# Performance work log

Measured on AMD Instinct MI355X. Metric: run time of the kernel, lower is better.

## Reference

```python
import jax, jax.numpy as jnp
import numpy as np

EMBED_DIM = 768
NUM_HEADS = 12
HEAD_DIM = EMBED_DIM // NUM_HEADS
B, T = 2, 2048


def setup_inputs() -> dict:
    key = jax.random.key(0)
    ks = jax.random.split(key, 11)
    s = 1.0 / np.sqrt(EMBED_DIM)
    return {
        "query": jax.random.normal(ks[0], (B, T, EMBED_DIM), jnp.float32),
        "key_in": jax.random.normal(ks[1], (B, T, EMBED_DIM), jnp.float32),
        "value": jax.random.normal(ks[2], (B, T, EMBED_DIM), jnp.float32),
        "Wq": jax.random.uniform(ks[3], (EMBED_DIM, EMBED_DIM), jnp.float32, -s, s),
        "bq": jnp.zeros((EMBED_DIM,), jnp.float32),
        "Wk": jax.random.uniform(ks[4], (EMBED_DIM, EMBED_DIM), jnp.float32, -s, s),
        "bk": jnp.zeros((EMBED_DIM,), jnp.float32),
        "Wv": jax.random.uniform(ks[5], (EMBED_DIM, EMBED_DIM), jnp.float32, -s, s),
        "bv": jnp.zeros((EMBED_DIM,), jnp.float32),
        "Wo": jax.random.uniform(ks[6], (EMBED_DIM, EMBED_DIM), jnp.float32, -s, s),
        "bo": jnp.zeros((EMBED_DIM,), jnp.float32),
    }


def reference(query, key_in, value, Wq, bq, Wk, bk, Wv, bv, Wo, bo):
    b, t, _ = query.shape

    def split_heads(x):  # [B,T,E] -> [B,H,T,Dh]
        return x.reshape(b, t, NUM_HEADS, HEAD_DIM).transpose(0, 2, 1, 3)

    Q = split_heads(query @ Wq + bq)
    K = split_heads(key_in @ Wk + bk)
    V = split_heads(value @ Wv + bv)

    scores = jnp.einsum("bhqd,bhkd->bhqk", Q, K) / np.sqrt(HEAD_DIM).astype(np.float32)
    attn = jax.nn.softmax(scores, axis=-1)
    out = jnp.einsum("bhqk,bhkd->bhqd", attn, V)  # [B,H,T,Dh]
    out = out.transpose(0, 2, 1, 3).reshape(b, t, EMBED_DIM)
    return out @ Wo + bo
```

## Files before the change

kernel.cpp:

```cpp
#include <hip/hip_runtime.h>
#include <math.h>

typedef __attribute__((ext_vector_type(4))) float  floatx4;
typedef __attribute__((ext_vector_type(8))) short  short8;
typedef __attribute__((ext_vector_type(4))) short  short4v;
typedef __attribute__((ext_vector_type(8))) __bf16 bf16x8;

#define E_DIM 768
#define T_DIM 2048
#define N_B   2
#define N_H   12
#define H_D   64
#define M_TOT 4096

#define Q_SCALE 0.1803368801111204f

#if __has_builtin(__builtin_amdgcn_exp2f)
#define EXP2F(x) __builtin_amdgcn_exp2f(x)
#else
#define EXP2F(x) exp2f(x)
#endif
#if __has_builtin(__builtin_amdgcn_rcpf)
#define RCPF(x) __builtin_amdgcn_rcpf(x)
#else
#define RCPF(x) (1.0f / (x))
#endif

__device__ __forceinline__ unsigned short f32_to_bf16(float f) {
  unsigned int u = __float_as_uint(f);
  u += 0x7fffu + ((u >> 16) & 1u);
  return (unsigned short)(u >> 16);
}

__device__ __forceinline__ unsigned short f32_to_bf16_trunc(float f) {
  return (unsigned short)(__float_as_uint(f) >> 16);
}

__device__ __forceinline__ void gload_lds16(const unsigned short* g, unsigned short* l) {
  __builtin_amdgcn_global_load_lds(
      (const __attribute__((address_space(1))) unsigned int*)(const void*)g,
      (__attribute__((address_space(3))) unsigned int*)(void*)l, 16, 0, 0);
}

__global__ __launch_bounds__(256) void convert_x(const float* __restrict__ q,
                                                 const float* __restrict__ k,
                                                 const float* __restrict__ v,
                                                 unsigned short* __restrict__ Xb) {
  const int z = blockIdx.y;
  const float* src = (z == 0) ? q : (z == 1) ? k : v;
  size_t idx = ((size_t)blockIdx.x * 256 + threadIdx.x) * 4;
  float4 val = *reinterpret_cast<const float4*>(&src[idx]);
  short4v o;
  o[0] = (short)f32_to_bf16(val.x);
  o[1] = (short)f32_to_bf16(val.y);
  o[2] = (short)f32_to_bf16(val.z);
  o[3] = (short)f32_to_bf16(val.w);
  *reinterpret_cast<short4v*>(&Xb[(size_t)z * M_TOT * E_DIM + idx]) = o;
}

__global__ __launch_bounds__(256) void transpose_w4(const float* __restrict__ W0,
                                                    const float* __restrict__ W1,
                                                    const float* __restrict__ W2,
                                                    const float* __restrict__ W3,
                                                    unsigned short* __restrict__ Wt) {
  __shared__ float tile[32][33];
  const int z = blockIdx.z;
  const float* W = (z == 0) ? W0 : (z == 1) ? W1 : (z == 2) ? W2 : W3;
  unsigned short* dst = Wt + (size_t)z * E_DIM * E_DIM;
  int k0 = blockIdx.x * 32, n0 = blockIdx.y * 32;
  int tx = threadIdx.x & 31, ty = threadIdx.x >> 5;
  for (int i = 0; i < 4; i++)
    tile[ty + i * 8][tx] = W[(size_t)(k0 + ty + i * 8) * E_DIM + n0 + tx];
  __syncthreads();
  for (int i = 0; i < 4; i++)
    dst[(size_t)(n0 + ty + i * 8) * E_DIM + k0 + tx] = f32_to_bf16(tile[tx][ty + i * 8]);
}

__global__ __launch_bounds__(256) void gemm_qkv(const unsigned short* __restrict__ Xb,
                                                const unsigned short* __restrict__ WtAll,
                                                const float* __restrict__ bq,
                                                const float* __restrict__ bk,
                                                const float* __restrict__ bv,
                                                unsigned short* __restrict__ outQKV) {
  __shared__ unsigned short As[128 * 32];
  __shared__ unsigned short Bs[128 * 32];

  const int z = blockIdx.z;
  const unsigned short* A = Xb + (size_t)z * M_TOT * E_DIM;
  const float* bias = (z == 0) ? bq : (z == 1) ? bk : bv;
  const unsigned short* W = WtAll + (size_t)z * E_DIM * E_DIM;
  unsigned short* out = outQKV + (size_t)z * M_TOT * E_DIM;
  const float scale = (z == 0) ? Q_SCALE : 1.0f;

  const int tid = threadIdx.x;
  const int lane = tid & 63, wv = tid >> 6;
  const int m15 = lane & 15, quad = lane >> 4;
  const int wm = (wv & 1) * 64, wn = (wv >> 1) * 64;
  const int m0 = blockIdx.x * 128, n0 = blockIdx.y * 128;

  floatx4 acc[4][4] = {};
  const int srow = lane >> 2, scol = (lane & 3) * 8;

  for (int k0 = 0; k0 < E_DIM; k0 += 32) {
    for (int cc = 0; cc < 2; cc++) {
      int c = wv * 2 + cc;
      gload_lds16(&A[(size_t)(m0 + c * 16 + srow) * E_DIM + k0 + scol], &As[c * 512]);
      gload_lds16(&W[(size_t)(n0 + c * 16 + srow) * E_DIM + k0 + scol], &Bs[c * 512]);
    }
    __syncthreads();
    bf16x8 af[4], bfr[4];
    for (int i = 0; i < 4; i++)
      af[i] = *reinterpret_cast<const bf16x8*>(&As[(wm + i * 16 + m15) * 32 + quad * 8]);
    for (int j = 0; j < 4; j++)
      bfr[j] = *reinterpret_cast<const bf16x8*>(&Bs[(wn + j * 16 + m15) * 32 + quad * 8]);
    for (int i = 0; i < 4; i++)
      for (int j = 0; j < 4; j++)
        acc[i][j] = __builtin_amdgcn_mfma_f32_16x16x32_bf16(af[i], bfr[j], acc[i][j], 0, 0, 0);
    __syncthreads();
  }

  for (int i = 0; i < 4; i++)
    for (int j = 0; j < 4; j++) {
      int gn = n0 + wn + j * 16 + m15;
      int h = gn >> 6, d = gn & 63;
      float bso = bias[gn];
      for (int r = 0; r < 4; r++) {
        int gm = m0 + wm + i * 16 + quad * 4 + r;
        int bb = gm >> 11, tt = gm & 2047;
        float v = (acc[i][j][r] + bso) * scale;
        out[(((size_t)bb * N_H + h) * T_DIM + tt) * H_D + d] = f32_to_bf16(v);
      }
    }
}

__global__ __launch_bounds__(256) void transpose_v(const unsigned short* __restrict__ Vg_all,
                                                   unsigned short* __restrict__ VT) {
  __shared__ unsigned short tile[64 * 72];
  const int t0 = blockIdx.x * 64, h = blockIdx.y, bb = blockIdx.z;
  const unsigned short* Vg = Vg_all + (((size_t)bb * N_H + h) * T_DIM) * H_D;
  unsigned short* VTh = VT + (((size_t)bb * N_H + h) * H_D) * T_DIM;
  const int tid = threadIdx.x;
  const int tloc = tid & 63, d0 = (tid >> 6) * 16;

  short8 r0 = *reinterpret_cast<const short8*>(&Vg[(size_t)(t0 + tloc) * H_D + d0]);
  short8 r1 = *reinterpret_cast<const short8*>(&Vg[(size_t)(t0 + tloc) * H_D + d0 + 8]);
#pragma unroll
  for (int j = 0; j < 8; j++) {
    tile[(d0 + j) * 72 + tloc] = (unsigned short)r0[j];
    tile[(d0 + 8 + j) * 72 + tloc] = (unsigned short)r1[j];
  }
  __syncthreads();
  const int d = tid >> 2, ts = (tid & 3) * 16;
  short8 w0 = *reinterpret_cast<const short8*>(&tile[d * 72 + ts]);
  short8 w1 = *reinterpret_cast<const short8*>(&tile[d * 72 + ts + 8]);
  *reinterpret_cast<short8*>(&VTh[(size_t)d * T_DIM + t0 + ts]) = w0;
  *reinterpret_cast<short8*>(&VTh[(size_t)d * T_DIM + t0 + ts + 8]) = w1;
}

__global__ __launch_bounds__(64) void attn(const unsigned short* __restrict__ QKV,
                                           const unsigned short* __restrict__ VT,
                                           unsigned short* __restrict__ ctx) {
  __shared__ unsigned short strip[32 * 72];

  const int qw = blockIdx.x, h = blockIdx.y, bb = blockIdx.z;
  const size_t headoff = (((size_t)bb * N_H + h) * T_DIM) * H_D;
  const unsigned short* Qg = QKV + headoff;
  const unsigned short* Kg = QKV + (size_t)M_TOT * E_DIM + headoff;
  const unsigned short* VTg = VT + (((size_t)bb * N_H + h) * H_D) * T_DIM;

  const int lane = threadIdx.x;
  const int m15 = lane & 15, quad = lane >> 4;
  const int q0 = qw * 32;

  const unsigned short* kbase = Kg + (size_t)(m15 * 64 + quad * 8);
  const unsigned short* vbase = VTg + (size_t)(m15 * 2048 + quad * 8);

#define KFRAG(kt, j, kk) \
  (*reinterpret_cast<const short8*>(kbase + (size_t)(kt) * 4096 + (j) * 1024 + (kk) * 32))
#define VFRAG(kt, j, kk) \
  (*reinterpret_cast<const short8*>(vbase + (size_t)(j) * 32768 + (kt) * 64 + (kk) * 32))

  bf16x8 aq[2][2];
  for (int g = 0; g < 2; g++)
    for (int kk = 0; kk < 2; kk++)
      aq[g][kk] = __builtin_bit_cast(bf16x8, *reinterpret_cast<const short8*>(
          &Qg[(size_t)(q0 + g * 16 + m15) * 64 + kk * 32 + quad * 8]));

  short8 kf[2][8], vf[2][8];
#pragma unroll
  for (int j = 0; j < 4; j++)
    for (int kk = 0; kk < 2; kk++) {
      kf[0][j * 2 + kk] = KFRAG(0, j, kk);
      vf[0][j * 2 + kk] = VFRAG(0, j, kk);
    }
#pragma unroll
  for (int j = 0; j < 4; j++)
    for (int kk = 0; kk < 2; kk++) {
      kf[1][j * 2 + kk] = KFRAG(1, j, kk);
      vf[1][j * 2 + kk] = VFRAG(1, j, kk);
    }

  floatx4 o[2][4] = {};
  floatx4 lacc[2] = {};
  const short8 ones_s = {0x3f80, 0x3f80, 0x3f80, 0x3f80, 0x3f80, 0x3f80, 0x3f80, 0x3f80};
  const bf16x8 onesb = __builtin_bit_cast(bf16x8, ones_s);

  for (int g = 0; g < 2; g++) {
    floatx4 s[4] = {};
    for (int kk = 0; kk < 2; kk++)
      for (int j = 0; j < 4; j++)
        s[j] = __builtin_amdgcn_mfma_f32_16x16x32_bf16(
            aq[g][kk], __builtin_bit_cast(bf16x8, kf[0][j * 2 + kk]), s[j], 0, 0, 0);
    for (int j = 0; j < 4; j++)
      for (int r = 0; r < 4; r++)
        strip[(g * 16 + quad * 4 + r) * 72 + j * 16 + m15] = f32_to_bf16_trunc(EXP2F(s[j][r]));
  }
#pragma unroll
  for (int j = 0; j < 4; j++)
    for (int kk = 0; kk < 2; kk++) kf[0][j * 2 + kk] = KFRAG(2, j, kk);
  asm volatile("s_waitcnt lgkmcnt(0)" ::: "memory");

#pragma unroll 2
  for (int kt = 1; kt < 32; kt++) {
    const int cp = kt & 1, pp = cp ^ 1;

    for (int g = 0; g < 2; g++)
      for (int kk = 0; kk < 2; kk++) {
        bf16x8 a = *reinterpret_cast<const bf16x8*>(&strip[(g * 16 + m15) * 72 + kk * 32 + quad * 8]);
        lacc[g] = __builtin_amdgcn_mfma_f32_16x16x32_bf16(a, onesb, lacc[g], 0, 0, 0);
        for (int j = 0; j < 4; j++)
          o[g][j] = __builtin_amdgcn_mfma_f32_16x16x32_bf16(
              a, __builtin_bit_cast(bf16x8, vf[pp][j * 2 + kk]), o[g][j], 0, 0, 0);
      }

    floatx4 s0[4] = {}, s1[4] = {};
    for (int kk = 0; kk < 2; kk++)
      for (int j = 0; j < 4; j++) {
        bf16x8 b = __builtin_bit_cast(bf16x8, kf[cp][j * 2 + kk]);
        s0[j] = __builtin_amdgcn_mfma_f32_16x16x32_bf16(aq[0][kk], b, s0[j], 0, 0, 0);
        s1[j] = __builtin_amdgcn_mfma_f32_16x16x32_bf16(aq[1][kk], b, s1[j], 0, 0, 0);
      }

    if (kt < 30)
#pragma unroll
      for (int j = 0; j < 4; j++)
        for (int kk = 0; kk < 2; kk++) kf[cp][j * 2 + kk] = KFRAG(kt + 2, j, kk);
    if (kt < 31)
#pragma unroll
      for (int j = 0; j < 4; j++)
        for (int kk = 0; kk < 2; kk++) vf[pp][j * 2 + kk] = VFRAG(kt + 1, j, kk);

    for (int j = 0; j < 4; j++)
      for (int r = 0; r < 4; r++) {
        strip[(quad * 4 + r) * 72 + j * 16 + m15] = f32_to_bf16_trunc(EXP2F(s0[j][r]));
        strip[(16 + quad * 4 + r) * 72 + j * 16 + m15] = f32_to_bf16_trunc(EXP2F(s1[j][r]));
      }
    asm volatile("s_waitcnt lgkmcnt(0)" ::: "memory");
  }

  for (int g = 0; g < 2; g++)
    for (int kk = 0; kk < 2; kk++) {
      bf16x8 a = *reinterpret_cast<const bf16x8*>(&strip[(g * 16 + m15) * 72 + kk * 32 + quad * 8]);
      lacc[g] = __builtin_amdgcn_mfma_f32_16x16x32_bf16(a, onesb, lacc[g], 0, 0, 0);
      for (int j = 0; j < 4; j++)
        o[g][j] = __builtin_amdgcn_mfma_f32_16x16x32_bf16(
            a, __builtin_bit_cast(bf16x8, vf[1][j * 2 + kk]), o[g][j], 0, 0, 0);
    }

  for (int g = 0; g < 2; g++)
    for (int r = 0; r < 4; r++) {
      float rl = RCPF(lacc[g][r]);
      int q = q0 + g * 16 + quad * 4 + r;
      for (int j = 0; j < 4; j++)
        ctx[(size_t)(bb * T_DIM + q) * E_DIM + h * 64 + j * 16 + m15] =
            f32_to_bf16(o[g][j][r] * rl);
    }
#undef KFRAG
#undef VFRAG
}

__global__ __launch_bounds__(256) void gemm_out(const unsigned short* __restrict__ Actx,
                                                const unsigned short* __restrict__ Wt,
                                                const float* __restrict__ bias,
                                                float* __restrict__ out) {
  __shared__ unsigned short As[64 * 32];
  __shared__ unsigned short Bs[128 * 32];

  const int tid = threadIdx.x;
  const int lane = tid & 63, wv = tid >> 6;
  const int m15 = lane & 15, quad = lane >> 4;
  const int wm = (wv & 1) * 32, wn = (wv >> 1) * 64;
  const int m0 = blockIdx.x * 64, n0 = blockIdx.y * 128;

  floatx4 acc[2][4] = {};
  const int srow = lane >> 2, scol = (lane & 3) * 8;

  for (int k0 = 0; k0 < E_DIM; k0 += 32) {
    gload_lds16(&Actx[(size_t)(m0 + wv * 16 + srow) * E_DIM + k0 + scol], &As[wv * 512]);
    for (int cc = 0; cc < 2; cc++) {
      int c = wv * 2 + cc;
      gload_lds16(&Wt[(size_t)(n0 + c * 16 + srow) * E_DIM + k0 + scol], &Bs[c * 512]);
    }
    __syncthreads();
    bf16x8 af[2], bfr[4];
    for (int i = 0; i < 2; i++)
      af[i] = *reinterpret_cast<const bf16x8*>(&As[(wm + i * 16 + m15) * 32 + quad * 8]);
    for (int j = 0; j < 4; j++)
      bfr[j] = *reinterpret_cast<const bf16x8*>(&Bs[(wn + j * 16 + m15) * 32 + quad * 8]);
    for (int i = 0; i < 2; i++)
      for (int j = 0; j < 4; j++)
        acc[i][j] = __builtin_amdgcn_mfma_f32_16x16x32_bf16(af[i], bfr[j], acc[i][j], 0, 0, 0);
    __syncthreads();
  }

  for (int i = 0; i < 2; i++)
    for (int j = 0; j < 4; j++) {
      int gn = n0 + wn + j * 16 + m15;
      float bso = bias[gn];
      for (int r = 0; r < 4; r++) {
        int gm = m0 + wm + i * 16 + quad * 4 + r;
        out[(size_t)gm * E_DIM + gn] = acc[i][j][r] + bso;
      }
    }
}

extern "C" void kernel_launch(void* const* d_in, const int* in_sizes, int n_in,
                              void* d_out, int out_size, void* d_ws, size_t ws_size,
                              hipStream_t stream) {
  const float* query  = (const float*)d_in[0];
  const float* key_in = (const float*)d_in[1];
  const float* value  = (const float*)d_in[2];
  const float* Wq = (const float*)d_in[3];
  const float* bq = (const float*)d_in[4];
  const float* Wk = (const float*)d_in[5];
  const float* bk = (const float*)d_in[6];
  const float* Wv = (const float*)d_in[7];
  const float* bv = (const float*)d_in[8];
  const float* Wo = (const float*)d_in[9];
  const float* bo = (const float*)d_in[10];
  float* out = (float*)d_out;

  unsigned short* ws  = (unsigned short*)d_ws;
  unsigned short* Wt  = ws;
  unsigned short* Xb  = Wt + (size_t)4 * E_DIM * E_DIM;
  unsigned short* QKV = Xb + (size_t)3 * M_TOT * E_DIM;
  unsigned short* VT  = QKV + (size_t)3 * M_TOT * E_DIM;
  unsigned short* ctx = VT + (size_t)N_B * N_H * H_D * T_DIM;

  dim3 tb(256);
  convert_x<<<dim3(M_TOT * E_DIM / 1024, 3), tb, 0, stream>>>(query, key_in, value, Xb);
  transpose_w4<<<dim3(24, 24, 4), tb, 0, stream>>>(Wq, Wk, Wv, Wo, Wt);

  gemm_qkv<<<dim3(32, 6, 3), tb, 0, stream>>>(Xb, Wt, bq, bk, bv, QKV);
  transpose_v<<<dim3(32, 12, 2), tb, 0, stream>>>(QKV + (size_t)2 * M_TOT * E_DIM, VT);
  attn<<<dim3(64, 12, 2), dim3(64), 0, stream>>>(QKV, VT, ctx);
  gemm_out<<<dim3(64, 6), tb, 0, stream>>>(ctx, Wt + (size_t)3 * E_DIM * E_DIM, bo, out);
  (void)in_sizes; (void)n_in; (void)out_size; (void)ws_size;
}
```

Measured before the change: 239.4 us.

## Fuse prep kernels, write V transposed from QKV GEMM, restructure attention with LDS K tiles

The input conversion and weight-transpose kernels become one launch. The QKV GEMM epilogue writes V straight into the transposed layout, so the separate transpose_v kernel goes away. Attention now runs four waves per block: two query sub-tiles times two key splits. The block shares double-buffered, XOR-swizzled K tiles in LDS loaded with global_load_lds, and the two key halves are reduced through LDS at the end. This cuts launch count and redundant per-wave K loads, at the cost of block barriers each iteration and an extra reduction step.

```diff
diff --git a/kernel.cpp b/kernel.cpp
--- a/kernel.cpp
+++ b/kernel.cpp
@@ -42,38 +42,41 @@
       (__attribute__((address_space(3))) unsigned int*)(void*)l, 16, 0, 0);
 }
 
-__global__ __launch_bounds__(256) void convert_x(const float* __restrict__ q,
-                                                 const float* __restrict__ k,
-                                                 const float* __restrict__ v,
-                                                 unsigned short* __restrict__ Xb) {
-  const int z = blockIdx.y;
-  const float* src = (z == 0) ? q : (z == 1) ? k : v;
-  size_t idx = ((size_t)blockIdx.x * 256 + threadIdx.x) * 4;
-  float4 val = *reinterpret_cast<const float4*>(&src[idx]);
-  short4v o;
-  o[0] = (short)f32_to_bf16(val.x);
-  o[1] = (short)f32_to_bf16(val.y);
-  o[2] = (short)f32_to_bf16(val.z);
-  o[3] = (short)f32_to_bf16(val.w);
-  *reinterpret_cast<short4v*>(&Xb[(size_t)z * M_TOT * E_DIM + idx]) = o;
-}
-
-__global__ __launch_bounds__(256) void transpose_w4(const float* __restrict__ W0,
-                                                    const float* __restrict__ W1,
-                                                    const float* __restrict__ W2,
-                                                    const float* __restrict__ W3,
-                                                    unsigned short* __restrict__ Wt) {
+__global__ __launch_bounds__(256) void prep(const float* __restrict__ q,
+                                            const float* __restrict__ k,
+                                            const float* __restrict__ v,
+                                            const float* __restrict__ W0,
+                                            const float* __restrict__ W1,
+                                            const float* __restrict__ W2,
+                                            const float* __restrict__ W3,
+                                            unsigned short* __restrict__ Xb,
+                                            unsigned short* __restrict__ Wt) {
   __shared__ float tile[32][33];
-  const int z = blockIdx.z;
-  const float* W = (z == 0) ? W0 : (z == 1) ? W1 : (z == 2) ? W2 : W3;
-  unsigned short* dst = Wt + (size_t)z * E_DIM * E_DIM;
-  int k0 = blockIdx.x * 32, n0 = blockIdx.y * 32;
-  int tx = threadIdx.x & 31, ty = threadIdx.x >> 5;
-  for (int i = 0; i < 4; i++)
-    tile[ty + i * 8][tx] = W[(size_t)(k0 + ty + i * 8) * E_DIM + n0 + tx];
-  __syncthreads();
-  for (int i = 0; i < 4; i++)
-    dst[(size_t)(n0 + ty + i * 8) * E_DIM + k0 + tx] = f32_to_bf16(tile[tx][ty + i * 8]);
+  const int bx = blockIdx.x;
+  if (bx < 9216) {
+    const int z = bx / 3072, inner = bx % 3072;
+    const float* src = (z == 0) ? q : (z == 1) ? k : v;
+    size_t idx = ((size_t)inner * 256 + threadIdx.x) * 4;
+    float4 val = *reinterpret_cast<const float4*>(&src[idx]);
+    short4v o;
+    o[0] = (short)f32_to_bf16(val.x);
+    o[1] = (short)f32_to_bf16(val.y);
+    o[2] = (short)f32_to_bf16(val.z);
+    o[3] = (short)f32_to_bf16(val.w);
+    *reinterpret_cast<short4v*>(&Xb[(size_t)z * M_TOT * E_DIM + idx]) = o;
+  } else {
+    const int t = bx - 9216;
+    const int z = t / 576, rem = t % 576;
+    const float* W = (z == 0) ? W0 : (z == 1) ? W1 : (z == 2) ? W2 : W3;
+    unsigned short* dst = Wt + (size_t)z * E_DIM * E_DIM;
+    int k0 = (rem / 24) * 32, n0 = (rem % 24) * 32;
+    int tx = threadIdx.x & 31, ty = threadIdx.x >> 5;
+    for (int i = 0; i < 4; i++)
+      tile[ty + i * 8][tx] = W[(size_t)(k0 + ty + i * 8) * E_DIM + n0 + tx];
+    __syncthreads();
+    for (int i = 0; i < 4; i++)
+      dst[(size_t)(n0 + ty + i * 8) * E_DIM + k0 + tx] = f32_to_bf16(tile[tx][ty + i * 8]);
+  }
 }
 
 __global__ __launch_bounds__(256) void gemm_qkv(const unsigned short* __restrict__ Xb,
@@ -81,7 +84,8 @@
                                                 const float* __restrict__ bq,
                                                 const float* __restrict__ bk,
                                                 const float* __restrict__ bv,
-                                                unsigned short* __restrict__ outQKV) {
+                                                unsigned short* __restrict__ outQKV,
+                                                unsigned short* __restrict__ VTout) {
   __shared__ unsigned short As[128 * 32];
   __shared__ unsigned short Bs[128 * 32];
 
@@ -119,66 +123,68 @@
     __syncthreads();
   }
 
-  for (int i = 0; i < 4; i++)
-    for (int j = 0; j < 4; j++) {
-      int gn = n0 + wn + j * 16 + m15;
-      int h = gn >> 6, d = gn & 63;
-      float bso = bias[gn];
-      for (int r = 0; r < 4; r++) {
-        int gm = m0 + wm + i * 16 + quad * 4 + r;
-        int bb = gm >> 11, tt = gm & 2047;
-        float v = (acc[i][j][r] + bso) * scale;
-        out[(((size_t)bb * N_H + h) * T_DIM + tt) * H_D + d] = f32_to_bf16(v);
-      }
-    }
-}
-
-__global__ __launch_bounds__(256) void transpose_v(const unsigned short* __restrict__ Vg_all,
-                                                   unsigned short* __restrict__ VT) {
-  __shared__ unsigned short tile[64 * 72];
-  const int t0 = blockIdx.x * 64, h = blockIdx.y, bb = blockIdx.z;
-  const unsigned short* Vg = Vg_all + (((size_t)bb * N_H + h) * T_DIM) * H_D;
-  unsigned short* VTh = VT + (((size_t)bb * N_H + h) * H_D) * T_DIM;
-  const int tid = threadIdx.x;
-  const int tloc = tid & 63, d0 = (tid >> 6) * 16;
-
-  short8 r0 = *reinterpret_cast<const short8*>(&Vg[(size_t)(t0 + tloc) * H_D + d0]);
-  short8 r1 = *reinterpret_cast<const short8*>(&Vg[(size_t)(t0 + tloc) * H_D + d0 + 8]);
-#pragma unroll
-  for (int j = 0; j < 8; j++) {
-    tile[(d0 + j) * 72 + tloc] = (unsigned short)r0[j];
-    tile[(d0 + 8 + j) * 72 + tloc] = (unsigned short)r1[j];
-  }
-  __syncthreads();
-  const int d = tid >> 2, ts = (tid & 3) * 16;
-  short8 w0 = *reinterpret_cast<const short8*>(&tile[d * 72 + ts]);
-  short8 w1 = *reinterpret_cast<const short8*>(&tile[d * 72 + ts + 8]);
-  *reinterpret_cast<short8*>(&VTh[(size_t)d * T_DIM + t0 + ts]) = w0;
-  *reinterpret_cast<short8*>(&VTh[(size_t)d * T_DIM + t0 + ts + 8]) = w1;
-}
-
-__global__ __launch_bounds__(64) void attn(const unsigned short* __restrict__ QKV,
-                                           const unsigned short* __restrict__ VT,
-                                           unsigned short* __restrict__ ctx) {
-  __shared__ unsigned short strip[32 * 72];
-
-  const int qw = blockIdx.x, h = blockIdx.y, bb = blockIdx.z;
+  if (z == 2) {
+    for (int i = 0; i < 4; i++)
+      for (int j = 0; j < 4; j++) {
+        int gn = n0 + wn + j * 16 + m15;
+        int hh = gn >> 6, d = gn & 63;
+        float bso = bias[gn];
+        int gm0 = m0 + wm + i * 16 + quad * 4;
+        int bb2 = gm0 >> 11, t0 = gm0 & 2047;
+        unsigned int d0 = ((unsigned int)f32_to_bf16(acc[i][j][1] + bso) << 16) |
+                          f32_to_bf16(acc[i][j][0] + bso);
+        unsigned int d1 = ((unsigned int)f32_to_bf16(acc[i][j][3] + bso) << 16) |
+                          f32_to_bf16(acc[i][j][2] + bso);
+        uint2 dd; dd.x = d0; dd.y = d1;
+        *reinterpret_cast<uint2*>(
+            &VTout[(((size_t)bb2 * N_H + hh) * H_D + d) * T_DIM + t0]) = dd;
+      }
+  } else {
+    for (int i = 0; i < 4; i++)
+      for (int j = 0; j < 4; j++) {
+        int gn = n0 + wn + j * 16 + m15;
+        int h = gn >> 6, d = gn & 63;
+        float bso = bias[gn];
+        for (int r = 0; r < 4; r++) {
+          int gm = m0 + wm + i * 16 + quad * 4 + r;
+          int bb = gm >> 11, tt = gm & 2047;
+          float vv = (acc[i][j][r] + bso) * scale;
+          out[(((size_t)bb * N_H + h) * T_DIM + tt) * H_D + d] = f32_to_bf16(vv);
+        }
+      }
+  }
+}
+
+__global__ __launch_bounds__(256) void attn(const unsigned short* __restrict__ QKV,
+                                            const unsigned short* __restrict__ VT,
+                                            unsigned short* __restrict__ ctx) {
+  __shared__ unsigned short Kbuf[2][2][64 * 64];
+  __shared__ unsigned short strips[4][32 * 72];
+
+  const int qb = blockIdx.x, h = blockIdx.y, bb = blockIdx.z;
   const size_t headoff = (((size_t)bb * N_H + h) * T_DIM) * H_D;
   const unsigned short* Qg = QKV + headoff;
   const unsigned short* Kg = QKV + (size_t)M_TOT * E_DIM + headoff;
   const unsigned short* VTg = VT + (((size_t)bb * N_H + h) * H_D) * T_DIM;
 
-  const int lane = threadIdx.x;
+  const int tid = threadIdx.x, lane = tid & 63, wv = tid >> 6;
   const int m15 = lane & 15, quad = lane >> 4;
-  const int q0 = qw * 32;
-
-  const unsigned short* kbase = Kg + (size_t)(m15 * 64 + quad * 8);
-  const unsigned short* vbase = VTg + (size_t)(m15 * 2048 + quad * 8);
-
-#define KFRAG(kt, j, kk) \
-  (*reinterpret_cast<const short8*>(kbase + (size_t)(kt) * 4096 + (j) * 1024 + (kk) * 32))
-#define VFRAG(kt, j, kk) \
-  (*reinterpret_cast<const short8*>(vbase + (size_t)(j) * 32768 + (kt) * 64 + (kk) * 32))
+  const int qs = wv & 1, ks = wv >> 1;
+  const int q0 = qb * 64 + qs * 32;
+
+  auto stage = [&](int t0, int ping) {
+#pragma unroll
+    for (int i = 0; i < 4; i++) {
+      int c = tid + i * 256;
+      int tile = c >> 9, cc = c & 511;
+      int key = cc >> 3, dc = cc & 7;
+      int dcs = dc ^ (key & 7);
+      gload_lds16(&Kg[((size_t)(t0 + tile) * 64 + key) * 64 + dcs * 8],
+                  &Kbuf[ping][tile][cc * 8]);
+    }
+  };
+
+  stage(0, 0);
 
   bf16x8 aq[2][2];
   for (int g = 0; g < 2; g++)
@@ -186,97 +192,94 @@
       aq[g][kk] = __builtin_bit_cast(bf16x8, *reinterpret_cast<const short8*>(
           &Qg[(size_t)(q0 + g * 16 + m15) * 64 + kk * 32 + quad * 8]));
 
-  short8 kf[2][8], vf[2][8];
-#pragma unroll
-  for (int j = 0; j < 4; j++)
-    for (int kk = 0; kk < 2; kk++) {
-      kf[0][j * 2 + kk] = KFRAG(0, j, kk);
-      vf[0][j * 2 + kk] = VFRAG(0, j, kk);
-    }
-#pragma unroll
-  for (int j = 0; j < 4; j++)
-    for (int kk = 0; kk < 2; kk++) {
-      kf[1][j * 2 + kk] = KFRAG(1, j, kk);
-      vf[1][j * 2 + kk] = VFRAG(1, j, kk);
-    }
+  const unsigned short* vbase = VTg + (size_t)(m15 * 2048 + quad * 8);
+#define VFRAG(kt, nt, kk2) \
+  (*reinterpret_cast<const short8*>(vbase + (size_t)(nt) * 32768 + (kt) * 64 + (kk2) * 32))
+
+  short8 vf[8];
+#pragma unroll
+  for (int nt = 0; nt < 4; nt++)
+    for (int kk2 = 0; kk2 < 2; kk2++) vf[nt * 2 + kk2] = VFRAG(ks, nt, kk2);
 
   floatx4 o[2][4] = {};
   floatx4 lacc[2] = {};
   const short8 ones_s = {0x3f80, 0x3f80, 0x3f80, 0x3f80, 0x3f80, 0x3f80, 0x3f80, 0x3f80};
   const bf16x8 onesb = __builtin_bit_cast(bf16x8, ones_s);
-
-  for (int g = 0; g < 2; g++) {
-    floatx4 s[4] = {};
+  unsigned short* strip = strips[wv];
+
+  for (int r = 0; r < 16; r++) {
+    __syncthreads();
+    if (r < 15) stage(2 * r + 2, (r + 1) & 1);
+    const unsigned short* Kt = Kbuf[r & 1][ks];
+    const int kt = 2 * r + ks;
+
+    floatx4 s[2][4] = {};
     for (int kk = 0; kk < 2; kk++)
-      for (int j = 0; j < 4; j++)
-        s[j] = __builtin_amdgcn_mfma_f32_16x16x32_bf16(
-            aq[g][kk], __builtin_bit_cast(bf16x8, kf[0][j * 2 + kk]), s[j], 0, 0, 0);
-    for (int j = 0; j < 4; j++)
-      for (int r = 0; r < 4; r++)
-        strip[(g * 16 + quad * 4 + r) * 72 + j * 16 + m15] = f32_to_bf16_trunc(EXP2F(s[j][r]));
-  }
-#pragma unroll
-  for (int j = 0; j < 4; j++)
-    for (int kk = 0; kk < 2; kk++) kf[0][j * 2 + kk] = KFRAG(2, j, kk);
-  asm volatile("s_waitcnt lgkmcnt(0)" ::: "memory");
-
-#pragma unroll 2
-  for (int kt = 1; kt < 32; kt++) {
-    const int cp = kt & 1, pp = cp ^ 1;
+#pragma unroll
+      for (int mt = 0; mt < 4; mt++) {
+        bf16x8 a = *reinterpret_cast<const bf16x8*>(
+            &Kt[(mt * 16 + m15) * 64 + (((kk * 4 + quad) ^ (m15 & 7)) * 8)]);
+        s[0][mt] = __builtin_amdgcn_mfma_f32_16x16x32_bf16(a, aq[0][kk], s[0][mt], 0, 0, 0);
+        s[1][mt] = __builtin_amdgcn_mfma_f32_16x16x32_bf16(a, aq[1][kk], s[1][mt], 0, 0, 0);
+      }
 
     for (int g = 0; g < 2; g++)
-      for (int kk = 0; kk < 2; kk++) {
-        bf16x8 a = *reinterpret_cast<const bf16x8*>(&strip[(g * 16 + m15) * 72 + kk * 32 + quad * 8]);
+#pragma unroll
+      for (int mt = 0; mt < 4; mt++) {
+        unsigned int d0 = ((unsigned int)f32_to_bf16_trunc(EXP2F(s[g][mt][1])) << 16) |
+                          f32_to_bf16_trunc(EXP2F(s[g][mt][0]));
+        unsigned int d1 = ((unsigned int)f32_to_bf16_trunc(EXP2F(s[g][mt][3])) << 16) |
+                          f32_to_bf16_trunc(EXP2F(s[g][mt][2]));
+        uint2 dd; dd.x = d0; dd.y = d1;
+        *reinterpret_cast<uint2*>(&strip[(g * 16 + m15) * 72 + mt * 16 + quad * 4]) = dd;
+      }
+    asm volatile("s_waitcnt lgkmcnt(0)" ::: "memory");
+
+    for (int kk2 = 0; kk2 < 2; kk2++)
+      for (int g = 0; g < 2; g++) {
+        bf16x8 a = *reinterpret_cast<const bf16x8*>(
+            &strip[(g * 16 + m15) * 72 + kk2 * 32 + quad * 8]);
         lacc[g] = __builtin_amdgcn_mfma_f32_16x16x32_bf16(a, onesb, lacc[g], 0, 0, 0);
-        for (int j = 0; j < 4; j++)
-          o[g][j] = __builtin_amdgcn_mfma_f32_16x16x32_bf16(
-              a, __builtin_bit_cast(bf16x8, vf[pp][j * 2 + kk]), o[g][j], 0, 0, 0);
-      }
-
-    floatx4 s0[4] = {}, s1[4] = {};
-    for (int kk = 0; kk < 2; kk++)
-      for (int j = 0; j < 4; j++) {
-        bf16x8 b = __builtin_bit_cast(bf16x8, kf[cp][j * 2 + kk]);
-        s0[j] = __builtin_amdgcn_mfma_f32_16x16x32_bf16(aq[0][kk], b, s0[j], 0, 0, 0);
-        s1[j] = __builtin_amdgcn_mfma_f32_16x16x32_bf16(aq[1][kk], b, s1[j], 0, 0, 0);
-      }
-
-    if (kt < 30)
-#pragma unroll
-      for (int j = 0; j < 4; j++)
-        for (int kk = 0; kk < 2; kk++) kf[cp][j * 2 + kk] = KFRAG(kt + 2, j, kk);
-    if (kt < 31)
-#pragma unroll
-      for (int j = 0; j < 4; j++)
-        for (int kk = 0; kk < 2; kk++) vf[pp][j * 2 + kk] = VFRAG(kt + 1, j, kk);
-
-    for (int j = 0; j < 4; j++)
-      for (int r = 0; r < 4; r++) {
-        strip[(quad * 4 + r) * 72 + j * 16 + m15] = f32_to_bf16_trunc(EXP2F(s0[j][r]));
-        strip[(16 + quad * 4 + r) * 72 + j * 16 + m15] = f32_to_bf16_trunc(EXP2F(s1[j][r]));
-      }
-    asm volatile("s_waitcnt lgkmcnt(0)" ::: "memory");
-  }
-
-  for (int g = 0; g < 2; g++)
-    for (int kk = 0; kk < 2; kk++) {
-      bf16x8 a = *reinterpret_cast<const bf16x8*>(&strip[(g * 16 + m15) * 72 + kk * 32 + quad * 8]);
-      lacc[g] = __builtin_amdgcn_mfma_f32_16x16x32_bf16(a, onesb, lacc[g], 0, 0, 0);
-      for (int j = 0; j < 4; j++)
-        o[g][j] = __builtin_amdgcn_mfma_f32_16x16x32_bf16(
-            a, __builtin_bit_cast(bf16x8, vf[1][j * 2 + kk]), o[g][j], 0, 0, 0);
-    }
-
-  for (int g = 0; g < 2; g++)
-    for (int r = 0; r < 4; r++) {
-      float rl = RCPF(lacc[g][r]);
-      int q = q0 + g * 16 + quad * 4 + r;
-      for (int j = 0; j < 4; j++)
-        ctx[(size_t)(bb * T_DIM + q) * E_DIM + h * 64 + j * 16 + m15] =
-            f32_to_bf16(o[g][j][r] * rl);
-    }
-#undef KFRAG
+#pragma unroll
+        for (int nt = 0; nt < 4; nt++)
+          o[g][nt] = __builtin_amdgcn_mfma_f32_16x16x32_bf16(
+              a, __builtin_bit_cast(bf16x8, vf[nt * 2 + kk2]), o[g][nt], 0, 0, 0);
+      }
+
+    if (r < 15)
+#pragma unroll
+      for (int nt = 0; nt < 4; nt++)
+        for (int kk2 = 0; kk2 < 2; kk2++) vf[nt * 2 + kk2] = VFRAG(kt + 2, nt, kk2);
+  }
 #undef VFRAG
+
+  __syncthreads();
+  float* red = (float*)&Kbuf[0][0][0];
+  if (ks == 1) {
+    floatx4* dst = (floatx4*)(red + (size_t)(qs * 64 + lane) * 40);
+#pragma unroll
+    for (int g = 0; g < 2; g++)
+      for (int nt = 0; nt < 4; nt++) dst[g * 4 + nt] = o[g][nt];
+    dst[8] = lacc[0];
+    dst[9] = lacc[1];
+  }
+  __syncthreads();
+  if (ks == 0) {
+    const floatx4* src = (const floatx4*)(red + (size_t)(qs * 64 + lane) * 40);
+#pragma unroll
+    for (int g = 0; g < 2; g++)
+      for (int nt = 0; nt < 4; nt++) o[g][nt] += src[g * 4 + nt];
+    lacc[0] += src[8];
+    lacc[1] += src[9];
+    for (int g = 0; g < 2; g++)
+      for (int r4 = 0; r4 < 4; r4++) {
+        float rl = RCPF(lacc[g][r4]);
+        int qq = q0 + g * 16 + quad * 4 + r4;
+        for (int nt = 0; nt < 4; nt++)
+          ctx[(size_t)(bb * T_DIM + qq) * E_DIM + h * 64 + nt * 16 + m15] =
+              f32_to_bf16(o[g][nt][r4] * rl);
+      }
+  }
 }
 
 __global__ __launch_bounds__(256) void gemm_out(const unsigned short* __restrict__ Actx,
@@ -348,12 +351,9 @@
   unsigned short* ctx = VT + (size_t)N_B * N_H * H_D * T_DIM;
 
   dim3 tb(256);
-  convert_x<<<dim3(M_TOT * E_DIM / 1024, 3), tb, 0, stream>>>(query, key_in, value, Xb);
-  transpose_w4<<<dim3(24, 24, 4), tb, 0, stream>>>(Wq, Wk, Wv, Wo, Wt);
-
-  gemm_qkv<<<dim3(32, 6, 3), tb, 0, stream>>>(Xb, Wt, bq, bk, bv, QKV);
-  transpose_v<<<dim3(32, 12, 2), tb, 0, stream>>>(QKV + (size_t)2 * M_TOT * E_DIM, VT);
-  attn<<<dim3(64, 12, 2), dim3(64), 0, stream>>>(QKV, VT, ctx);
+  prep<<<dim3(11520), tb, 0, stream>>>(query, key_in, value, Wq, Wk, Wv, Wo, Xb, Wt);
+  gemm_qkv<<<dim3(32, 6, 3), tb, 0, stream>>>(Xb, Wt, bq, bk, bv, QKV, VT);
+  attn<<<dim3(32, 12, 2), tb, 0, stream>>>(QKV, VT, ctx);
   gemm_out<<<dim3(64, 6), tb, 0, stream>>>(ctx, Wt + (size_t)3 * E_DIM * E_DIM, bo, out);
   (void)in_sizes; (void)n_in; (void)out_size; (void)ws_size;
 }
```

Measured after the change: 213.7 us. 1.12x faster.
